# Performance work log

Measured on AMD Instinct MI355X. Metric: run time of the kernel, lower is better.

The kernel has to match this reference:

```python
import jax, jax.numpy as jnp
import numpy as np

N, E, H, L = 20000, 640000, 128, 3
IN_NODE, IN_EDGE = 128, 128


def _ln(x):
    m = jnp.mean(x, -1, keepdims=True)
    v = jnp.mean((x - m) ** 2, -1, keepdims=True)
    return (x - m) / jnp.sqrt(v + 1e-5)


def _multi_aggr(msg, dst, n):
    # PyG MultiAggregation(['mean','std','max','min']) -> concat on feature dim
    cnt = jax.ops.segment_sum(jnp.ones((msg.shape[0],), msg.dtype), dst, n)
    denom = jnp.maximum(cnt, 1.0)[:, None]
    mean = jax.ops.segment_sum(msg, dst, n) / denom
    mean2 = jax.ops.segment_sum(msg * msg, dst, n) / denom
    std = jnp.sqrt(jax.nn.relu(mean2 - mean * mean) + 1e-5)  # PyG StdAggregation
    has = (cnt > 0)[:, None]
    mx = jnp.where(has, jax.ops.segment_max(msg, dst, n), 0.0)
    mn = jnp.where(has, jax.ops.segment_min(msg, dst, n), 0.0)
    return jnp.concatenate([mean, std, mx, mn], axis=-1)  # [n, 4H]


def _pna(h, src, dst, ea, W1, b1, W2, b2, W3, b3, W4, b4, Wd, bd, n):
    # flow='source_to_target': j = src = edge_index[0], i = dst = edge_index[1]
    x1 = jax.nn.silu(h @ W1 + b1)  # lin1 -> x_j
    z = jax.nn.silu(h @ W2 + b2)   # lin2 -> z_i
    msg = z[dst] * x1[src] * ea    # message = z_i * x_j * edge_attr
    ret_node = _multi_aggr(msg, dst, n) @ Wd + bd
    ret_edge = jax.nn.silu(h @ W3 + b3)[src] * jax.nn.silu(h @ W4 + b4)[dst] * ea
    return ret_node, ret_edge


def _gnn(x, edge_index, edge_attr, Wn, bn, We, be, W1, b1, W2, b2, W3, b3, W4, b4,
         Wd, bd, Wnd1, bnd1, Wnd2, bnd2, Wed1, bed1, Wed2, bed2):
    n = x.shape[0]
    h = Wn.shape[1]
    src, dst = edge_index[0], edge_index[1]
    inv = jnp.concatenate([jnp.ones((h // 2,), x.dtype), -jnp.ones(((h + 1) // 2,), x.dtype)])
    hidden = x @ Wn + bn
    in_ea = edge_attr
    ea = edge_attr @ We + be
    for i in range(W1.shape[0]):
        hn = _ln(hidden)
        rn1, re1 = _pna(hn, src, dst, ea, W1[i], b1[i], W2[i], b2[i], W3[i], b3[i], W4[i], b4[i], Wd[i], bd[i], n)
        rn2, re2 = _pna(hn, dst, src, inv * ea, W1[i], b1[i], W2[i], b2[i], W3[i], b3[i], W4[i], b4[i], Wd[i], bd[i], n)
        hidden = hidden + rn1 + rn2
        ea = ea + re1 + inv * re2
    node_pred = x + 0.01 * (jax.nn.silu(_ln(hidden) @ Wnd1 + bnd1) @ Wnd2 + bnd2)
    edge_pred = in_ea + 0.01 * (jax.nn.silu(_ln(ea) @ Wed1 + bed1) @ Wed2 + bed2)
    return node_pred, edge_pred


def setup_inputs() -> dict:
    key = jax.random.key(0)
    ks = jax.random.split(key, 20)
    g = lambda k, s, sc=0.05: jax.random.normal(k, s, jnp.float32) * sc
    return {
        "x": g(ks[0], (N, IN_NODE), 1.0),
        "edge_attr": g(ks[1], (E, IN_EDGE), 1.0),
        "Wn": g(ks[2], (IN_NODE, H)), "bn": jnp.zeros((H,), jnp.float32),
        "We": g(ks[3], (IN_EDGE, H)), "be": jnp.zeros((H,), jnp.float32),
        "W1": g(ks[4], (L, H, H)), "b1": jnp.zeros((L, H), jnp.float32),
        "W2": g(ks[5], (L, H, H)), "b2": jnp.zeros((L, H), jnp.float32),
        "W3": g(ks[6], (L, H, H)), "b3": jnp.zeros((L, H), jnp.float32),
        "W4": g(ks[7], (L, H, H)), "b4": jnp.zeros((L, H), jnp.float32),
        "Wd": g(ks[8], (L, 4 * H, H)), "bd": jnp.zeros((L, H), jnp.float32),
        "Wnd1": g(ks[9], (H, H)), "bnd1": jnp.zeros((H,), jnp.float32),
        "Wnd2": g(ks[10], (H, IN_NODE)), "bnd2": jnp.zeros((IN_NODE,), jnp.float32),
        "Wed1": g(ks[11], (H, H)), "bed1": jnp.zeros((H,), jnp.float32),
        "Wed2": g(ks[12], (H, IN_EDGE)), "bed2": jnp.zeros((IN_EDGE,), jnp.float32),
        "edge_index": jax.random.randint(ks[13], (2, E), 0, N),
    }


def reference(x, edge_attr, Wn, bn, We, be, W1, b1, W2, b2, W3, b3, W4, b4, Wd, bd,
              Wnd1, bnd1, Wnd2, bnd2, Wed1, bed1, Wed2, bed2, edge_index):
    return _gnn(x, edge_index, edge_attr, Wn, bn, We, be, W1, b1, W2, b2, W3, b3,
                W4, b4, Wd, bd, Wnd1, bnd1, Wnd2, bnd2, Wed1, bed1, Wed2, bed2)
```

## Files before the change

kernel.cpp:

```cpp
#include <hip/hip_runtime.h>
#include <cstdint>
#include <cstddef>

typedef __attribute__((ext_vector_type(8))) short short8x;
typedef __attribute__((ext_vector_type(4))) float f32x4;

static constexpr int NN = 20000;
static constexpr int EE = 640000;
static constexpr int NT_E = EE / 128;

#define DEVI __device__ __forceinline__

DEVI float b2f(uint16_t u){ union{uint32_t i; float f;} x; x.i = (uint32_t)u<<16; return x.f; }
DEVI uint16_t f2b(float f){ union{float f; uint32_t i;} x; x.f=f; uint32_t i=x.i;
  return (uint16_t)((i + 0x7FFFu + ((i>>16)&1u))>>16); }
DEVI float silu_f(float v){ return v / (1.f + __expf(-v)); }

DEVI uint4 pack8(float4 a, float4 b){
  union{uint16_t u[8]; uint4 q;} pk;
  pk.u[0]=f2b(a.x); pk.u[1]=f2b(a.y); pk.u[2]=f2b(a.z); pk.u[3]=f2b(a.w);
  pk.u[4]=f2b(b.x); pk.u[5]=f2b(b.y); pk.u[6]=f2b(b.z); pk.u[7]=f2b(b.w);
  return pk.q;
}
DEVI uint2 pack4(float4 a){
  union{uint16_t u[4]; uint2 q;} pk;
  pk.u[0]=f2b(a.x); pk.u[1]=f2b(a.y); pk.u[2]=f2b(a.z); pk.u[3]=f2b(a.w);
  return pk.q;
}
DEVI float4 unpk4(uint2 v){
  return (float4){ b2f((uint16_t)(v.x & 0xFFFFu)), b2f((uint16_t)(v.x >> 16)),
                   b2f((uint16_t)(v.y & 0xFFFFu)), b2f((uint16_t)(v.y >> 16)) };
}
DEVI short8x pk_frag(float4 a, float4 b){
  union{uint16_t u[8]; short8x s;} pk;
  pk.u[0]=f2b(a.x); pk.u[1]=f2b(a.y); pk.u[2]=f2b(a.z); pk.u[3]=f2b(a.w);
  pk.u[4]=f2b(b.x); pk.u[5]=f2b(b.y); pk.u[6]=f2b(b.z); pk.u[7]=f2b(b.w);
  return pk.s;
}

template<typename EAT>
DEVI void load8e(const EAT* base, size_t row, int col8, float4& a, float4& b){
  if constexpr (sizeof(EAT)==2){
    uint4 v = *(const uint4*)((const uint16_t*)base + row*128 + col8);
    a = (float4){b2f((uint16_t)(v.x&0xFFFFu)), b2f((uint16_t)(v.x>>16)),
                 b2f((uint16_t)(v.y&0xFFFFu)), b2f((uint16_t)(v.y>>16))};
    b = (float4){b2f((uint16_t)(v.z&0xFFFFu)), b2f((uint16_t)(v.z>>16)),
                 b2f((uint16_t)(v.w&0xFFFFu)), b2f((uint16_t)(v.w>>16))};
  } else {
    const float* f = (const float*)base + row*128 + col8;
    a = *(const float4*)f; b = *(const float4*)(f+4);
  }
}
template<typename EAT>
DEVI void store4e(EAT* base, size_t idx, float4 v){
  if constexpr (sizeof(EAT)==2) *(uint2*)((uint16_t*)base + idx) = pack4(v);
  else *(float4*)((float*)base + idx) = v;
}
template<typename EAT>
DEVI float4 ld4e(const EAT* base, size_t idx){
  if constexpr (sizeof(EAT)==2) return unpk4(*(const uint2*)((const uint16_t*)base + idx));
  else return *(const float4*)((const float*)base + idx);
}

DEVI void ln8(float4& a, float4& b){
  float s = a.x+a.y+a.z+a.w + b.x+b.y+b.z+b.w;
  float q = a.x*a.x+a.y*a.y+a.z*a.z+a.w*a.w + b.x*b.x+b.y*b.y+b.z*b.z+b.w*b.w;
#pragma unroll
  for (int d=1; d<16; d<<=1){ s += __shfl_xor(s,d); q += __shfl_xor(q,d); }
  float m = s * 0.0078125f;
  float rstd = rsqrtf(fmaxf(q*0.0078125f - m*m, 0.f) + 1e-5f);
  a.x=(a.x-m)*rstd; a.y=(a.y-m)*rstd; a.z=(a.z-m)*rstd; a.w=(a.w-m)*rstd;
  b.x=(b.x-m)*rstd; b.y=(b.y-m)*rstd; b.z=(b.z-m)*rstd; b.w=(b.w-m)*rstd;
}

template<int AF32, int LNA, int EPI, int SILU>
__global__ __launch_bounds__(256) void gemm_node(
    const void* Ap, const uint16_t* __restrict__ Wt,
    const float* __restrict__ bias, float bias_scale,
    int M, int K,
    uint16_t* outb, float* outf,
    const float* __restrict__ resid, float resid_scale)
{
  __shared__ uint16_t Als[128*136];
  __shared__ uint16_t Wls[128*136];
  const int t = threadIdx.x;
  const int row0 = blockIdx.x * 128;
  const int w = t >> 6, l = t & 63;
  const int lr = l & 15, lk = (l>>4)*8;

  f32x4 acc[2][8];
#pragma unroll
  for (int a=0;a<2;a++)
#pragma unroll
    for(int b=0;b<8;b++) acc[a][b] = (f32x4){0.f,0.f,0.f,0.f};

  for (int kc = 0; kc < K; kc += 128){
#pragma unroll
    for (int i=0;i<8;i++){
      int c = t + i*256;
      int r = c >> 4, k8 = (c & 15)*8;
      int gr = row0 + r;
      if (AF32){
        float4 a = {0.f,0.f,0.f,0.f}, b = {0.f,0.f,0.f,0.f};
        if (gr < M){
          const float* Af = (const float*)Ap + (size_t)gr*K + kc + k8;
          a = *(const float4*)Af; b = *(const float4*)(Af + 4);
        }
        if (LNA) ln8(a, b);
        *(uint4*)(&Als[r*136 + k8]) = pack8(a, b);
      } else {
        uint4 v = {0u,0u,0u,0u};
        if (gr < M) v = *(const uint4*)((const uint16_t*)Ap + (size_t)gr*K + kc + k8);
        *(uint4*)(&Als[r*136 + k8]) = v;
      }
    }
#pragma unroll
    for (int i=0;i<8;i++){
      int c = t + i*256;
      int r = c >> 4, k8 = (c & 15)*8;
      *(uint4*)(&Wls[r*136 + k8]) = *(const uint4*)(Wt + (size_t)r*K + kc + k8);
    }
    __syncthreads();
#pragma unroll
    for (int kt=0; kt<4; ++kt){
      int kb = kt*32 + lk;
      short8x bfr[8];
#pragma unroll
      for (int c16=0;c16<8;c16++) bfr[c16] = *(const short8x*)(&Wls[(c16*16+lr)*136 + kb]);
#pragma unroll
      for (int r16=0;r16<2;r16++){
        short8x afr = *(const short8x*)(&Als[(w*32 + r16*16 + lr)*136 + kb]);
#pragma unroll
        for (int c16=0;c16<8;c16++)
          acc[r16][c16] = __builtin_amdgcn_mfma_f32_16x16x32_bf16(bfr[c16], afr, acc[r16][c16], 0,0,0);
      }
    }
    __syncthreads();
  }

  float4 bbv[8];
#pragma unroll
  for (int c16=0;c16<8;c16++){
    float4 b4 = *(const float4*)(bias + c16*16 + (l>>4)*4);
    bbv[c16] = (float4){b4.x*bias_scale, b4.y*bias_scale, b4.z*bias_scale, b4.w*bias_scale};
  }
#pragma unroll
  for (int r16=0;r16<2;r16++){
    int row = row0 + w*32 + r16*16 + lr;
    if (row >= M) continue;
#pragma unroll
    for (int c16=0;c16<8;c16++){
      int colb = c16*16 + (l>>4)*4;
      float4 v = (float4){acc[r16][c16][0]+bbv[c16].x, acc[r16][c16][1]+bbv[c16].y,
                          acc[r16][c16][2]+bbv[c16].z, acc[r16][c16][3]+bbv[c16].w};
      if (SILU){ v.x=silu_f(v.x); v.y=silu_f(v.y); v.z=silu_f(v.z); v.w=silu_f(v.w); }
      size_t o = (size_t)row*128 + colb;
      if (EPI==0)      *(uint2*)(outb + o) = pack4(v);
      else if (EPI==1) *(float4*)(outf + o) = v;
      else if (EPI==2){ float4 old = *(const float4*)(outf + o);
        *(float4*)(outf + o) = (float4){old.x+v.x, old.y+v.y, old.z+v.z, old.w+v.w}; }
      else { float4 r = *(const float4*)(resid + o);
        *(float4*)(outf + o) = (float4){r.x+resid_scale*v.x, r.y+resid_scale*v.y,
                                        r.z+resid_scale*v.z, r.w+resid_scale*v.w}; }
    }
  }
}

__global__ __launch_bounds__(256) void proj4(
    const float* __restrict__ hidden, const uint16_t* __restrict__ Wt4,
    const float* __restrict__ b0p, const float* __restrict__ b1p,
    const float* __restrict__ b2p, const float* __restrict__ b3p,
    uint16_t* o0, uint16_t* o1, uint16_t* o2, uint16_t* o3, int M)
{
  __shared__ uint16_t Als[128*136];
  __shared__ uint16_t Wls[2][128*136];
  const int t = threadIdx.x;
  const int row0 = blockIdx.x * 128;
  const int w = t >> 6, l = t & 63;
  const int lr = l & 15, lk = (l>>4)*8;

#pragma unroll
  for (int i=0;i<8;i++){
    int c = t + i*256;
    int r = c >> 4, k8 = (c & 15)*8;
    int gr = row0 + r;
    float4 a = {0.f,0.f,0.f,0.f}, b = {0.f,0.f,0.f,0.f};
    if (gr < M){
      const float* Af = hidden + (size_t)gr*128 + k8;
      a = *(const float4*)Af; b = *(const float4*)(Af + 4);
    }
    ln8(a, b);
    *(uint4*)(&Als[r*136 + k8]) = pack8(a, b);
  }
#pragma unroll
  for (int i=0;i<8;i++){
    int c = t + i*256;
    int r = c >> 4, k8 = (c & 15)*8;
    *(uint4*)(&Wls[0][r*136 + k8]) = *(const uint4*)(Wt4 + (size_t)r*128 + k8);
  }
  __syncthreads();

#pragma unroll
  for (int p=0; p<4; ++p){
    if (p < 3){
#pragma unroll
      for (int i=0;i<8;i++){
        int c = t + i*256;
        int r = c >> 4, k8 = (c & 15)*8;
        *(uint4*)(&Wls[(p+1)&1][r*136 + k8]) =
          *(const uint4*)(Wt4 + (size_t)(p+1)*16384 + (size_t)r*128 + k8);
      }
    }
    f32x4 acc[2][8];
#pragma unroll
    for (int a=0;a<2;a++)
#pragma unroll
      for(int b=0;b<8;b++) acc[a][b] = (f32x4){0.f,0.f,0.f,0.f};
#pragma unroll
    for (int kt=0; kt<4; ++kt){
      int kb = kt*32 + lk;
      short8x bfr[8];
#pragma unroll
      for (int c16=0;c16<8;c16++) bfr[c16] = *(const short8x*)(&Wls[p&1][(c16*16+lr)*136 + kb]);
#pragma unroll
      for (int r16=0;r16<2;r16++){
        short8x afr = *(const short8x*)(&Als[(w*32 + r16*16 + lr)*136 + kb]);
#pragma unroll
        for (int c16=0;c16<8;c16++)
          acc[r16][c16] = __builtin_amdgcn_mfma_f32_16x16x32_bf16(bfr[c16], afr, acc[r16][c16], 0,0,0);
      }
    }
    const float* bp = (p==0)?b0p:(p==1)?b1p:(p==2)?b2p:b3p;
    uint16_t* op = (p==0)?o0:(p==1)?o1:(p==2)?o2:o3;
#pragma unroll
    for (int r16=0;r16<2;r16++){
      int row = row0 + w*32 + r16*16 + lr;
      if (row >= M) continue;
#pragma unroll
      for (int c16=0;c16<8;c16++){
        int colb = c16*16 + (l>>4)*4;
        float4 b4 = *(const float4*)(bp + colb);
        float4 v = (float4){silu_f(acc[r16][c16][0]+b4.x), silu_f(acc[r16][c16][1]+b4.y),
                            silu_f(acc[r16][c16][2]+b4.z), silu_f(acc[r16][c16][3]+b4.w)};
        *(uint2*)(op + (size_t)row*128 + colb) = pack4(v);
      }
    }
    __syncthreads();
  }
}

template<typename EAT>
__global__ __launch_bounds__(256, 2) void enc_edge(
    const float* __restrict__ A, const uint16_t* __restrict__ Wt,
    const float* __restrict__ bias, EAT* __restrict__ out)
{
  const int t = threadIdx.x, w = t >> 6, l = t & 63;
  const int lr = l & 15, g = l >> 4;
  const size_t base = (size_t)blockIdx.x*128 + w*32;

  short8x fr[2][4];
#pragma unroll
  for (int r16=0;r16<2;r16++){
#pragma unroll
    for (int kt=0;kt<4;kt++){
      const float* Af = A + (base + r16*16 + lr)*128 + kt*32 + g*8;
      float4 a = *(const float4*)Af, b = *(const float4*)(Af + 4);
      fr[r16][kt] = pk_frag(a, b);
    }
  }
  f32x4 acc[2][8];
#pragma unroll
  for (int a=0;a<2;a++)
#pragma unroll
    for (int b=0;b<8;b++) acc[a][b] = (f32x4){0.f,0.f,0.f,0.f};
#pragma unroll
  for (int kt=0;kt<4;kt++){
#pragma unroll
    for (int c16=0;c16<8;c16++){
      short8x bfr = *(const short8x*)(Wt + (size_t)(c16*16+lr)*128 + kt*32 + g*8);
      acc[0][c16] = __builtin_amdgcn_mfma_f32_16x16x32_bf16(bfr, fr[0][kt], acc[0][c16], 0,0,0);
      acc[1][c16] = __builtin_amdgcn_mfma_f32_16x16x32_bf16(bfr, fr[1][kt], acc[1][c16], 0,0,0);
    }
  }
#pragma unroll
  for (int r16=0;r16<2;r16++){
    size_t row = base + r16*16 + lr;
#pragma unroll
    for (int c16=0;c16<8;c16++){
      int colb = c16*16 + g*4;
      float4 b4 = *(const float4*)(bias + colb);
      store4e(out, row*128 + colb,
        (float4){acc[r16][c16][0]+b4.x, acc[r16][c16][1]+b4.y,
                 acc[r16][c16][2]+b4.z, acc[r16][c16][3]+b4.w});
    }
  }
}

template<typename EAT>
__global__ __launch_bounds__(256, 2) void dec_edge(
    const EAT* ea, const float* __restrict__ eatt,
    const uint16_t* __restrict__ W1t, const uint16_t* __restrict__ W2t,
    const float* __restrict__ b1, const float* __restrict__ b2,
    float* outf)
{
  __shared__ uint16_t Pls[4][32*136];
  const int t = threadIdx.x, w = t >> 6, l = t & 63;
  const int lr = l & 15, g = l >> 4;
  uint16_t* Ps = &Pls[w][0];
  const size_t base = (size_t)blockIdx.x*128 + w*32;

  short8x fr[2][4];
#pragma unroll
  for (int r16=0;r16<2;r16++){
    float4 va[4][2];
    float s=0.f, q=0.f;
#pragma unroll
    for (int kt=0;kt<4;kt++){
      load8e(ea, base + r16*16 + lr, kt*32 + g*8, va[kt][0], va[kt][1]);
      float4 a = va[kt][0], b = va[kt][1];
      s += a.x+a.y+a.z+a.w + b.x+b.y+b.z+b.w;
      q += a.x*a.x+a.y*a.y+a.z*a.z+a.w*a.w + b.x*b.x+b.y*b.y+b.z*b.z+b.w*b.w;
    }
    s += __shfl_xor(s,16); q += __shfl_xor(q,16);
    s += __shfl_xor(s,32); q += __shfl_xor(q,32);
    float m = s*0.0078125f;
    float rstd = rsqrtf(fmaxf(q*0.0078125f - m*m, 0.f) + 1e-5f);
#pragma unroll
    for (int kt=0;kt<4;kt++){
      float4 a = va[kt][0], b = va[kt][1];
      a.x=(a.x-m)*rstd; a.y=(a.y-m)*rstd; a.z=(a.z-m)*rstd; a.w=(a.w-m)*rstd;
      b.x=(b.x-m)*rstd; b.y=(b.y-m)*rstd; b.z=(b.z-m)*rstd; b.w=(b.w-m)*rstd;
      fr[r16][kt] = pk_frag(a, b);
    }
  }
  f32x4 acc[2][8];
#pragma unroll
  for (int a=0;a<2;a++)
#pragma unroll
    for (int b=0;b<8;b++) acc[a][b] = (f32x4){0.f,0.f,0.f,0.f};
#pragma unroll
  for (int kt=0;kt<4;kt++){
#pragma unroll
    for (int c16=0;c16<8;c16++){
      short8x bfr = *(const short8x*)(W1t + (size_t)(c16*16+lr)*128 + kt*32 + g*8);
      acc[0][c16] = __builtin_amdgcn_mfma_f32_16x16x32_bf16(fr[0][kt], bfr, acc[0][c16], 0,0,0);
      acc[1][c16] = __builtin_amdgcn_mfma_f32_16x16x32_bf16(fr[1][kt], bfr, acc[1][c16], 0,0,0);
    }
  }
#pragma unroll
  for (int c16=0;c16<8;c16++){
    float bb = b1[c16*16+lr];
#pragma unroll
    for (int r16=0;r16<2;r16++)
#pragma unroll
      for (int j=0;j<4;j++)
        Ps[(r16*16 + g*4 + j)*136 + c16*16 + lr] = f2b(silu_f(acc[r16][c16][j] + bb));
  }
  f32x4 acc2[2][8];
#pragma unroll
  for (int a=0;a<2;a++)
#pragma unroll
    for (int b=0;b<8;b++) acc2[a][b] = (f32x4){0.f,0.f,0.f,0.f};
#pragma unroll
  for (int kt=0;kt<4;kt++){
    short8x a0 = *(const short8x*)(Ps + (0*16 + lr)*136 + kt*32 + g*8);
    short8x a1 = *(const short8x*)(Ps + (1*16 + lr)*136 + kt*32 + g*8);
#pragma unroll
    for (int c16=0;c16<8;c16++){
      short8x bfr = *(const short8x*)(W2t + (size_t)(c16*16+lr)*128 + kt*32 + g*8);
      acc2[0][c16] = __builtin_amdgcn_mfma_f32_16x16x32_bf16(bfr, a0, acc2[0][c16], 0,0,0);
      acc2[1][c16] = __builtin_amdgcn_mfma_f32_16x16x32_bf16(bfr, a1, acc2[1][c16], 0,0,0);
    }
  }
#pragma unroll
  for (int r16=0;r16<2;r16++){
    size_t row = base + r16*16 + lr;
    float4 et[8];
#pragma unroll
    for (int c16=0;c16<8;c16++) et[c16] = *(const float4*)(eatt + row*128 + c16*16 + g*4);
#pragma unroll
    for (int c16=0;c16<8;c16++){
      int colb = c16*16 + g*4;
      float4 bb = *(const float4*)(b2 + colb);
      *(float4*)(outf + row*128 + colb) =
        (float4){et[c16].x + 0.01f*(acc2[r16][c16][0]+bb.x),
                 et[c16].y + 0.01f*(acc2[r16][c16][1]+bb.y),
                 et[c16].z + 0.01f*(acc2[r16][c16][2]+bb.z),
                 et[c16].w + 0.01f*(acc2[r16][c16][3]+bb.w)};
    }
  }
}

template<typename EAT, int INV, int EUPD, int ACCUM>
__global__ __launch_bounds__(128) void agg_kernel(
    const EAT* ea, EAT* ea_out,
    const uint16_t* __restrict__ x1, const uint16_t* __restrict__ z,
    const uint16_t* __restrict__ h3, const uint16_t* __restrict__ h4,
    const int* __restrict__ eids, const int* __restrict__ ptr,
    const int* __restrict__ other, uint16_t* stats)
{
  __shared__ int se[128];
  __shared__ int so[128];
  __shared__ float red[4][4][128];
  const int i = blockIdx.x, t = threadIdx.x;
  const int g = t >> 5, q = t & 31;
  const int f0 = q*4;
  float4 zi = unpk4(*(const uint2*)(z + (size_t)i*128 + f0));
  float4 h3i = {0,0,0,0}, h4i = {0,0,0,0};
  if (EUPD){
    h3i = unpk4(*(const uint2*)(h3 + (size_t)i*128 + f0));
    h4i = unpk4(*(const uint2*)(h4 + (size_t)i*128 + f0));
  }
  const int beg = ptr[i], end = ptr[i+1];
  float4 s={0,0,0,0}, s2={0,0,0,0};
  float4 mx={-3.4e38f,-3.4e38f,-3.4e38f,-3.4e38f}, mn={3.4e38f,3.4e38f,3.4e38f,3.4e38f};
  for (int jb = beg; jb < end; jb += 128){
    int cn = min(128, end - jb);
    if (t < cn){ int e = eids[jb+t]; se[t] = e; so[t] = other[e]; }
    __syncthreads();
#pragma unroll 2
    for (int jj = g; jj < cn; jj += 4){
      int e = se[jj], o = so[jj];
      float4 xo = unpk4(*(const uint2*)(x1 + (size_t)o*128 + f0));
      float4 ev = ld4e(ea, (size_t)e*128 + f0);
      float4 m = (float4){zi.x*xo.x*ev.x, zi.y*xo.y*ev.y, zi.z*xo.z*ev.z, zi.w*xo.w*ev.w};
      if (INV){ if (q >= 16){ m.x=-m.x; m.y=-m.y; m.z=-m.z; m.w=-m.w; } }
      s.x+=m.x; s.y+=m.y; s.z+=m.z; s.w+=m.w;
      s2.x+=m.x*m.x; s2.y+=m.y*m.y; s2.z+=m.z*m.z; s2.w+=m.w*m.w;
      mx.x=fmaxf(mx.x,m.x); mx.y=fmaxf(mx.y,m.y); mx.z=fmaxf(mx.z,m.z); mx.w=fmaxf(mx.w,m.w);
      mn.x=fminf(mn.x,m.x); mn.y=fminf(mn.y,m.y); mn.z=fminf(mn.z,m.z); mn.w=fminf(mn.w,m.w);
      if (EUPD){
        float4 h3o = unpk4(*(const uint2*)(h3 + (size_t)o*128 + f0));
        float4 h4o = unpk4(*(const uint2*)(h4 + (size_t)o*128 + f0));
        store4e(ea_out, (size_t)e*128 + f0,
          (float4){ev.x*(1.f + h3o.x*h4i.x + h3i.x*h4o.x),
                   ev.y*(1.f + h3o.y*h4i.y + h3i.y*h4o.y),
                   ev.z*(1.f + h3o.z*h4i.z + h3i.z*h4o.z),
                   ev.w*(1.f + h3o.w*h4i.w + h3i.w*h4o.w)});
      }
    }
    __syncthreads();
  }
  *(float4*)(&red[g][0][f0]) = s;
  *(float4*)(&red[g][1][f0]) = s2;
  *(float4*)(&red[g][2][f0]) = mx;
  *(float4*)(&red[g][3][f0]) = mn;
  __syncthreads();
  float fs = red[0][0][t]+red[1][0][t]+red[2][0][t]+red[3][0][t];
  float fq = red[0][1][t]+red[1][1][t]+red[2][1][t]+red[3][1][t];
  float fmx = fmaxf(fmaxf(red[0][2][t],red[1][2][t]), fmaxf(red[2][2][t],red[3][2][t]));
  float fmn = fminf(fminf(red[0][3][t],red[1][3][t]), fminf(red[2][3][t],red[3][3][t]));
  int cnt = end - beg;
  float dn = cnt > 0 ? 1.f/(float)cnt : 1.f;
  float mean = fs*dn, m2 = fq*dn;
  float sd = sqrtf(fmaxf(m2 - mean*mean, 0.f) + 1e-5f);
  if (cnt == 0){ fmx = 0.f; fmn = 0.f; }
  size_t o0 = (size_t)i*512 + t;
  if (ACCUM){
    stats[o0    ] = f2b(b2f(stats[o0    ]) + mean);
    stats[o0+128] = f2b(b2f(stats[o0+128]) + sd);
    stats[o0+256] = f2b(b2f(stats[o0+256]) + fmx);
    stats[o0+384] = f2b(b2f(stats[o0+384]) + fmn);
  } else {
    stats[o0]=f2b(mean); stats[o0+128]=f2b(sd); stats[o0+256]=f2b(fmx); stats[o0+384]=f2b(fmn);
  }
}

__global__ void count_deg(const int* __restrict__ ei, int* cnt_src, int* cnt_dst){
  int e = blockIdx.x*256 + threadIdx.x;
  if (e < EE){
    atomicAdd(&cnt_src[ei[e]], 1);
    atomicAdd(&cnt_dst[ei[EE+e]], 1);
  }
}

__global__ __launch_bounds__(1024) void scan20k(const int* __restrict__ cnt, int* ptr){
  __shared__ int buf[1024];
  constexpr int C = 20;
  int t = threadIdx.x;
  int base = t*C;
  int loc[C];
  int sum = 0;
#pragma unroll
  for (int j=0;j<C;j++){
    int idx = base+j;
    int v = (idx < NN) ? cnt[idx] : 0;
    loc[j] = sum; sum += v;
  }
  buf[t] = sum;
  __syncthreads();
  for (int sft=1; sft<1024; sft<<=1){
    int add = (t>=sft) ? buf[t-sft] : 0;
    __syncthreads();
    buf[t] += add;
    __syncthreads();
  }
  int excl = buf[t] - sum;
#pragma unroll
  for (int j=0;j<C;j++){
    int idx = base+j;
    if (idx < NN) ptr[idx] = excl + loc[j];
  }
  if (t == 1023) ptr[NN] = buf[1023];
}

__global__ void init_cursor(const int* p1, int* c1, const int* p2, int* c2, int n){
  int i = blockIdx.x*256 + threadIdx.x;
  if (i < n){ c1[i] = p1[i]; c2[i] = p2[i]; }
}

__global__ void scatter_edges(const int* __restrict__ ei, int* cur_src, int* cur_dst,
                              int* eid_src, int* eid_dst){
  int e = blockIdx.x*256 + threadIdx.x;
  if (e < EE){
    int s = ei[e], d = ei[EE+e];
    eid_src[atomicAdd(&cur_src[s],1)] = e;
    eid_dst[atomicAdd(&cur_dst[d],1)] = e;
  }
}

__global__ void transpose_w(const float* __restrict__ W, uint16_t* __restrict__ Wt,
                            int K, int total, int ostride, int ooff){
  int idx = blockIdx.x*256 + threadIdx.x;
  if (idx < total){
    int per = K*128;
    int m = idx / per, r = idx - m*per;
    int k = r >> 7, c = r & 127;
    Wt[(size_t)m*ostride + ooff + (size_t)c*K + k] = f2b(W[idx]);
  }
}

extern "C" void kernel_launch(void* const* d_in, const int* in_sizes, int n_in,
                              void* d_out, int out_size, void* d_ws, size_t ws_size,
                              hipStream_t stream)
{
  const float* x    = (const float*)d_in[0];
  const float* eatt = (const float*)d_in[1];
  const float* Wn   = (const float*)d_in[2];
  const float* bn   = (const float*)d_in[3];
  const float* We   = (const float*)d_in[4];
  const float* be   = (const float*)d_in[5];
  const float* W1   = (const float*)d_in[6];
  const float* b1   = (const float*)d_in[7];
  const float* W2   = (const float*)d_in[8];
  const float* b2   = (const float*)d_in[9];
  const float* W3   = (const float*)d_in[10];
  const float* b3   = (const float*)d_in[11];
  const float* W4   = (const float*)d_in[12];
  const float* b4   = (const float*)d_in[13];
  const float* Wd   = (const float*)d_in[14];
  const float* bd   = (const float*)d_in[15];
  const float* Wnd1 = (const float*)d_in[16];
  const float* bnd1 = (const float*)d_in[17];
  const float* Wnd2 = (const float*)d_in[18];
  const float* bnd2 = (const float*)d_in[19];
  const float* Wed1 = (const float*)d_in[20];
  const float* bed1 = (const float*)d_in[21];
  const float* Wed2 = (const float*)d_in[22];
  const float* bed2 = (const float*)d_in[23];
  const int* ei     = (const int*)d_in[24];

  float* out_node = (float*)d_out;
  float* out_edge = out_node + (size_t)NN*128;

  char* p = (char*)d_ws;
  auto alloc = [&](size_t bytes)->char*{
    char* r = p; p += (bytes + 255) & ~(size_t)255; return r; };

  float*    hidden = (float*)   alloc((size_t)NN*128*4);
  uint16_t* x1b    = (uint16_t*)alloc((size_t)NN*128*2);
  uint16_t* zb     = (uint16_t*)alloc((size_t)NN*128*2);
  uint16_t* h3b    = (uint16_t*)alloc((size_t)NN*128*2);
  uint16_t* h4b    = (uint16_t*)alloc((size_t)NN*128*2);
  uint16_t* stats  = (uint16_t*)alloc((size_t)NN*512*2);
  int* cnt_src = (int*)alloc((size_t)NN*4);
  int* cnt_dst = (int*)alloc((size_t)NN*4);
  int* ptr_src = (int*)alloc((size_t)(NN+1)*4);
  int* ptr_dst = (int*)alloc((size_t)(NN+1)*4);
  int* cur_src = (int*)alloc((size_t)NN*4);
  int* cur_dst = (int*)alloc((size_t)NN*4);
  int* eid_src = (int*)alloc((size_t)EE*4);
  int* eid_dst = (int*)alloc((size_t)EE*4);
  uint16_t* WT  = (uint16_t*)alloc((size_t)294912*2);
  uint16_t* wp4 = (uint16_t*)alloc((size_t)3*65536*2);

  uint16_t* wnT   = WT;
  uint16_t* weT   = WT + 16384;
  uint16_t* wdT   = WT + 32768;
  uint16_t* wnd1T = WT + 229376;
  uint16_t* wnd2T = WT + 245760;
  uint16_t* wed1T = WT + 262144;
  uint16_t* wed2T = WT + 278528;

  size_t used = (size_t)(p - (char*)d_ws);
  bool ea16ok = (ws_size >= used + (size_t)EE*128*2 + 512);
  uint16_t* ea16 = nullptr;
  if (ea16ok) ea16 = (uint16_t*)alloc((size_t)EE*128*2);
  float* eaf = out_edge;

  hipMemsetAsync(cnt_src, 0, (size_t)NN*4, stream);
  hipMemsetAsync(cnt_dst, 0, (size_t)NN*4, stream);
  count_deg<<<(EE+255)/256, 256, 0, stream>>>(ei, cnt_src, cnt_dst);
  scan20k<<<1, 1024, 0, stream>>>(cnt_src, ptr_src);
  scan20k<<<1, 1024, 0, stream>>>(cnt_dst, ptr_dst);
  init_cursor<<<(NN+255)/256, 256, 0, stream>>>(ptr_src, cur_src, ptr_dst, cur_dst, NN);
  scatter_edges<<<(EE+255)/256, 256, 0, stream>>>(ei, cur_src, cur_dst, eid_src, eid_dst);

  transpose_w<<<64, 256, 0, stream>>>(Wn, wnT, 128, 16384, 16384, 0);
  transpose_w<<<64, 256, 0, stream>>>(We, weT, 128, 16384, 16384, 0);
  transpose_w<<<192, 256, 0, stream>>>(W1, wp4, 128, 49152, 65536, 0);
  transpose_w<<<192, 256, 0, stream>>>(W2, wp4, 128, 49152, 65536, 16384);
  transpose_w<<<192, 256, 0, stream>>>(W3, wp4, 128, 49152, 65536, 32768);
  transpose_w<<<192, 256, 0, stream>>>(W4, wp4, 128, 49152, 65536, 49152);
  transpose_w<<<768, 256, 0, stream>>>(Wd, wdT, 512, 196608, 65536, 0);
  transpose_w<<<64, 256, 0, stream>>>(Wnd1, wnd1T, 128, 16384, 16384, 0);
  transpose_w<<<64, 256, 0, stream>>>(Wnd2, wnd2T, 128, 16384, 16384, 0);
  transpose_w<<<64, 256, 0, stream>>>(Wed1, wed1T, 128, 16384, 16384, 0);
  transpose_w<<<64, 256, 0, stream>>>(Wed2, wed2T, 128, 16384, 16384, 0);

  const int gN = (NN+127)/128;

  gemm_node<1,0,1,0><<<gN, 256, 0, stream>>>(x, wnT, bn, 1.f, NN, 128, nullptr, hidden, nullptr, 0.f);

  if (ea16ok){
    enc_edge<uint16_t><<<NT_E, 256, 0, stream>>>(eatt, weT, be, ea16);
    for (int lyr = 0; lyr < 3; ++lyr){
      proj4<<<gN, 256, 0, stream>>>(hidden, wp4 + (size_t)lyr*65536,
                                    b1 + lyr*128, b2 + lyr*128, b3 + lyr*128, b4 + lyr*128,
                                    x1b, zb, h3b, h4b, NN);
      agg_kernel<uint16_t,1,0,0><<<NN, 128, 0, stream>>>(ea16, nullptr, x1b, zb, nullptr, nullptr,
                                                         eid_src, ptr_src, ei + EE, stats);
      agg_kernel<uint16_t,0,1,1><<<NN, 128, 0, stream>>>(ea16, ea16, x1b, zb, h3b, h4b,
                                                         eid_dst, ptr_dst, ei, stats);
      gemm_node<0,0,2,0><<<gN, 256, 0, stream>>>(stats, wdT + lyr*65536, bd + lyr*128, 2.f,
                                                 NN, 512, nullptr, hidden, nullptr, 0.f);
    }
  } else {
    enc_edge<float><<<NT_E, 256, 0, stream>>>(eatt, weT, be, eaf);
    for (int lyr = 0; lyr < 3; ++lyr){
      proj4<<<gN, 256, 0, stream>>>(hidden, wp4 + (size_t)lyr*65536,
                                    b1 + lyr*128, b2 + lyr*128, b3 + lyr*128, b4 + lyr*128,
                                    x1b, zb, h3b, h4b, NN);
      agg_kernel<float,1,0,0><<<NN, 128, 0, stream>>>(eaf, nullptr, x1b, zb, nullptr, nullptr,
                                                      eid_src, ptr_src, ei + EE, stats);
      agg_kernel<float,0,1,1><<<NN, 128, 0, stream>>>(eaf, eaf, x1b, zb, h3b, h4b,
                                                      eid_dst, ptr_dst, ei, stats);
      gemm_node<0,0,2,0><<<gN, 256, 0, stream>>>(stats, wdT + lyr*65536, bd + lyr*128, 2.f,
                                                 NN, 512, nullptr, hidden, nullptr, 0.f);
    }
  }

  gemm_node<1,1,0,1><<<gN, 256, 0, stream>>>(hidden, wnd1T, bnd1, 1.f, NN, 128, x1b, nullptr, nullptr, 0.f);
  gemm_node<0,0,3,0><<<gN, 256, 0, stream>>>(x1b, wnd2T, bnd2, 1.f, NN, 128, nullptr, out_node, x, 0.01f);

  if (ea16ok)
    dec_edge<uint16_t><<<NT_E, 256, 0, stream>>>(ea16, eatt, wed1T, wed2T, bed1, bed2, out_edge);
  else
    dec_edge<float><<<NT_E, 256, 0, stream>>>(eaf, eatt, wed1T, wed2T, bed1, bed2, out_edge);
}
```

Baseline: 1.401 ms.

## Persistent prefetching edge encoder, wider aggregation blocks, fused weight transposes and cursor init

The edge encoder becomes a persistent kernel over 1000 blocks that prefetches the next tile's inputs into registers while the current tile runs its MFMAs, with bias hoisted out of the loop. Aggregation blocks double to 256 threads (8 edge groups), and the final reduction is split so half the threads compute mean/std and half max/min. The eleven weight-transpose launches merge into one kernel, and cursor initialisation folds into the scan. The edge decoder also issues its residual loads early. The aim is lower launch overhead, better latency hiding and more parallelism in the gather-bound aggregation, at the cost of higher register use and more shared memory per aggregation block.

```diff
diff --git a/kernel.cpp b/kernel.cpp
--- a/kernel.cpp
+++ b/kernel.cpp
@@ -256,43 +256,65 @@
 {
   const int t = threadIdx.x, w = t >> 6, l = t & 63;
   const int lr = l & 15, g = l >> 4;
-  const size_t base = (size_t)blockIdx.x*128 + w*32;
-
-  short8x fr[2][4];
-#pragma unroll
-  for (int r16=0;r16<2;r16++){
+
+  float4 bbv[8];
+#pragma unroll
+  for (int c16=0;c16<8;c16++) bbv[c16] = *(const float4*)(bias + c16*16 + g*4);
+
+  int tile = blockIdx.x;
+  float4 va[16];
+#pragma unroll
+  for (int r16=0;r16<2;r16++)
 #pragma unroll
     for (int kt=0;kt<4;kt++){
-      const float* Af = A + (base + r16*16 + lr)*128 + kt*32 + g*8;
-      float4 a = *(const float4*)Af, b = *(const float4*)(Af + 4);
-      fr[r16][kt] = pk_frag(a, b);
-    }
-  }
-  f32x4 acc[2][8];
-#pragma unroll
-  for (int a=0;a<2;a++)
-#pragma unroll
-    for (int b=0;b<8;b++) acc[a][b] = (f32x4){0.f,0.f,0.f,0.f};
-#pragma unroll
-  for (int kt=0;kt<4;kt++){
-#pragma unroll
-    for (int c16=0;c16<8;c16++){
-      short8x bfr = *(const short8x*)(Wt + (size_t)(c16*16+lr)*128 + kt*32 + g*8);
-      acc[0][c16] = __builtin_amdgcn_mfma_f32_16x16x32_bf16(bfr, fr[0][kt], acc[0][c16], 0,0,0);
-      acc[1][c16] = __builtin_amdgcn_mfma_f32_16x16x32_bf16(bfr, fr[1][kt], acc[1][c16], 0,0,0);
-    }
-  }
-#pragma unroll
-  for (int r16=0;r16<2;r16++){
-    size_t row = base + r16*16 + lr;
-#pragma unroll
-    for (int c16=0;c16<8;c16++){
-      int colb = c16*16 + g*4;
-      float4 b4 = *(const float4*)(bias + colb);
-      store4e(out, row*128 + colb,
-        (float4){acc[r16][c16][0]+b4.x, acc[r16][c16][1]+b4.y,
-                 acc[r16][c16][2]+b4.z, acc[r16][c16][3]+b4.w});
-    }
+      const float* Af = A + ((size_t)tile*128 + w*32 + r16*16 + lr)*128 + kt*32 + g*8;
+      va[r16*8+kt*2]   = *(const float4*)Af;
+      va[r16*8+kt*2+1] = *(const float4*)(Af + 4);
+    }
+  while (tile < NT_E){
+    short8x fr[2][4];
+#pragma unroll
+    for (int r16=0;r16<2;r16++)
+#pragma unroll
+      for (int kt=0;kt<4;kt++)
+        fr[r16][kt] = pk_frag(va[r16*8+kt*2], va[r16*8+kt*2+1]);
+    int next = tile + (int)gridDim.x;
+    if (next < NT_E){
+#pragma unroll
+      for (int r16=0;r16<2;r16++)
+#pragma unroll
+        for (int kt=0;kt<4;kt++){
+          const float* Af = A + ((size_t)next*128 + w*32 + r16*16 + lr)*128 + kt*32 + g*8;
+          va[r16*8+kt*2]   = *(const float4*)Af;
+          va[r16*8+kt*2+1] = *(const float4*)(Af + 4);
+        }
+    }
+    f32x4 acc[2][8];
+#pragma unroll
+    for (int a=0;a<2;a++)
+#pragma unroll
+      for (int b=0;b<8;b++) acc[a][b] = (f32x4){0.f,0.f,0.f,0.f};
+#pragma unroll
+    for (int kt=0;kt<4;kt++){
+#pragma unroll
+      for (int c16=0;c16<8;c16++){
+        short8x bfr = *(const short8x*)(Wt + (size_t)(c16*16+lr)*128 + kt*32 + g*8);
+        acc[0][c16] = __builtin_amdgcn_mfma_f32_16x16x32_bf16(bfr, fr[0][kt], acc[0][c16], 0,0,0);
+        acc[1][c16] = __builtin_amdgcn_mfma_f32_16x16x32_bf16(bfr, fr[1][kt], acc[1][c16], 0,0,0);
+      }
+    }
+#pragma unroll
+    for (int r16=0;r16<2;r16++){
+      size_t row = (size_t)tile*128 + w*32 + r16*16 + lr;
+#pragma unroll
+      for (int c16=0;c16<8;c16++){
+        int colb = c16*16 + g*4;
+        store4e(out, row*128 + colb,
+          (float4){acc[r16][c16][0]+bbv[c16].x, acc[r16][c16][1]+bbv[c16].y,
+                   acc[r16][c16][2]+bbv[c16].z, acc[r16][c16][3]+bbv[c16].w});
+      }
+    }
+    tile = next;
   }
 }
 
@@ -309,6 +331,15 @@
   uint16_t* Ps = &Pls[w][0];
   const size_t base = (size_t)blockIdx.x*128 + w*32;
 
+  float4 et[16];
+#pragma unroll
+  for (int r16=0;r16<2;r16++){
+    size_t row = base + r16*16 + lr;
+#pragma unroll
+    for (int c16=0;c16<8;c16++)
+      et[r16*8+c16] = *(const float4*)(eatt + row*128 + c16*16 + g*4);
+  }
+
   short8x fr[2][4];
 #pragma unroll
   for (int r16=0;r16<2;r16++){
@@ -375,24 +406,22 @@
 #pragma unroll
   for (int r16=0;r16<2;r16++){
     size_t row = base + r16*16 + lr;
-    float4 et[8];
-#pragma unroll
-    for (int c16=0;c16<8;c16++) et[c16] = *(const float4*)(eatt + row*128 + c16*16 + g*4);
 #pragma unroll
     for (int c16=0;c16<8;c16++){
       int colb = c16*16 + g*4;
       float4 bb = *(const float4*)(b2 + colb);
+      float4 e = et[r16*8+c16];
       *(float4*)(outf + row*128 + colb) =
-        (float4){et[c16].x + 0.01f*(acc2[r16][c16][0]+bb.x),
-                 et[c16].y + 0.01f*(acc2[r16][c16][1]+bb.y),
-                 et[c16].z + 0.01f*(acc2[r16][c16][2]+bb.z),
-                 et[c16].w + 0.01f*(acc2[r16][c16][3]+bb.w)};
+        (float4){e.x + 0.01f*(acc2[r16][c16][0]+bb.x),
+                 e.y + 0.01f*(acc2[r16][c16][1]+bb.y),
+                 e.z + 0.01f*(acc2[r16][c16][2]+bb.z),
+                 e.w + 0.01f*(acc2[r16][c16][3]+bb.w)};
     }
   }
 }
 
 template<typename EAT, int INV, int EUPD, int ACCUM>
-__global__ __launch_bounds__(128) void agg_kernel(
+__global__ __launch_bounds__(256) void agg_kernel(
     const EAT* ea, EAT* ea_out,
     const uint16_t* __restrict__ x1, const uint16_t* __restrict__ z,
     const uint16_t* __restrict__ h3, const uint16_t* __restrict__ h4,
@@ -401,7 +430,7 @@
 {
   __shared__ int se[128];
   __shared__ int so[128];
-  __shared__ float red[4][4][128];
+  __shared__ float red[8][4][128];
   const int i = blockIdx.x, t = threadIdx.x;
   const int g = t >> 5, q = t & 31;
   const int f0 = q*4;
@@ -418,8 +447,8 @@
     int cn = min(128, end - jb);
     if (t < cn){ int e = eids[jb+t]; se[t] = e; so[t] = other[e]; }
     __syncthreads();
-#pragma unroll 2
-    for (int jj = g; jj < cn; jj += 4){
+#pragma unroll 4
+    for (int jj = g; jj < cn; jj += 8){
       int e = se[jj], o = so[jj];
       float4 xo = unpk4(*(const uint2*)(x1 + (size_t)o*128 + f0));
       float4 ev = ld4e(ea, (size_t)e*128 + f0);
@@ -446,23 +475,35 @@
   *(float4*)(&red[g][2][f0]) = mx;
   *(float4*)(&red[g][3][f0]) = mn;
   __syncthreads();
-  float fs = red[0][0][t]+red[1][0][t]+red[2][0][t]+red[3][0][t];
-  float fq = red[0][1][t]+red[1][1][t]+red[2][1][t]+red[3][1][t];
-  float fmx = fmaxf(fmaxf(red[0][2][t],red[1][2][t]), fmaxf(red[2][2][t],red[3][2][t]));
-  float fmn = fminf(fminf(red[0][3][t],red[1][3][t]), fminf(red[2][3][t],red[3][3][t]));
   int cnt = end - beg;
-  float dn = cnt > 0 ? 1.f/(float)cnt : 1.f;
-  float mean = fs*dn, m2 = fq*dn;
-  float sd = sqrtf(fmaxf(m2 - mean*mean, 0.f) + 1e-5f);
-  if (cnt == 0){ fmx = 0.f; fmn = 0.f; }
-  size_t o0 = (size_t)i*512 + t;
-  if (ACCUM){
-    stats[o0    ] = f2b(b2f(stats[o0    ]) + mean);
-    stats[o0+128] = f2b(b2f(stats[o0+128]) + sd);
-    stats[o0+256] = f2b(b2f(stats[o0+256]) + fmx);
-    stats[o0+384] = f2b(b2f(stats[o0+384]) + fmn);
+  if (t < 128){
+    int f = t;
+    float fs=0.f, fq=0.f;
+#pragma unroll
+    for (int gg=0; gg<8; ++gg){ fs += red[gg][0][f]; fq += red[gg][1][f]; }
+    float dn = cnt > 0 ? 1.f/(float)cnt : 1.f;
+    float mean = fs*dn;
+    float sd = sqrtf(fmaxf(fq*dn - mean*mean, 0.f) + 1e-5f);
+    size_t o0 = (size_t)i*512 + f;
+    if (ACCUM){
+      stats[o0    ] = f2b(b2f(stats[o0    ]) + mean);
+      stats[o0+128] = f2b(b2f(stats[o0+128]) + sd);
+    } else {
+      stats[o0] = f2b(mean); stats[o0+128] = f2b(sd);
+    }
   } else {
-    stats[o0]=f2b(mean); stats[o0+128]=f2b(sd); stats[o0+256]=f2b(fmx); stats[o0+384]=f2b(fmn);
+    int f = t - 128;
+    float fmx=-3.4e38f, fmn=3.4e38f;
+#pragma unroll
+    for (int gg=0; gg<8; ++gg){ fmx = fmaxf(fmx, red[gg][2][f]); fmn = fminf(fmn, red[gg][3][f]); }
+    if (cnt == 0){ fmx = 0.f; fmn = 0.f; }
+    size_t o0 = (size_t)i*512 + f;
+    if (ACCUM){
+      stats[o0+256] = f2b(b2f(stats[o0+256]) + fmx);
+      stats[o0+384] = f2b(b2f(stats[o0+384]) + fmn);
+    } else {
+      stats[o0+256] = f2b(fmx); stats[o0+384] = f2b(fmn);
+    }
   }
 }
 
@@ -474,7 +515,7 @@
   }
 }
 
-__global__ __launch_bounds__(1024) void scan20k(const int* __restrict__ cnt, int* ptr){
+__global__ __launch_bounds__(1024) void scan20k(const int* __restrict__ cnt, int* ptr, int* cur){
   __shared__ int buf[1024];
   constexpr int C = 20;
   int t = threadIdx.x;
@@ -499,14 +540,9 @@
 #pragma unroll
   for (int j=0;j<C;j++){
     int idx = base+j;
-    if (idx < NN) ptr[idx] = excl + loc[j];
+    if (idx < NN){ int v = excl + loc[j]; ptr[idx] = v; cur[idx] = v; }
   }
   if (t == 1023) ptr[NN] = buf[1023];
-}
-
-__global__ void init_cursor(const int* p1, int* c1, const int* p2, int* c2, int n){
-  int i = blockIdx.x*256 + threadIdx.x;
-  if (i < n){ c1[i] = p1[i]; c2[i] = p2[i]; }
 }
 
 __global__ void scatter_edges(const int* __restrict__ ei, int* cur_src, int* cur_dst,
@@ -519,15 +555,21 @@
   }
 }
 
-__global__ void transpose_w(const float* __restrict__ W, uint16_t* __restrict__ Wt,
-                            int K, int total, int ostride, int ooff){
+struct TD { const float* s; uint16_t* d; int K; int ostride; int ooff; int cum; };
+struct TPack { TD td[11]; };
+__global__ __launch_bounds__(256) void transpose_all(TPack P, int total){
   int idx = blockIdx.x*256 + threadIdx.x;
-  if (idx < total){
-    int per = K*128;
-    int m = idx / per, r = idx - m*per;
-    int k = r >> 7, c = r & 127;
-    Wt[(size_t)m*ostride + ooff + (size_t)c*K + k] = f2b(W[idx]);
-  }
+  if (idx >= total) return;
+  int s = 0;
+#pragma unroll
+  for (int k=0;k<11;k++) s += (idx >= P.td[k].cum) ? 1 : 0;
+  int start = (s==0) ? 0 : P.td[s-1].cum;
+  int local = idx - start;
+  const TD& D = P.td[s];
+  int per = D.K*128;
+  int m = local / per, r = local - m*per;
+  int k = r >> 7, c = r & 127;
+  D.d[(size_t)m*D.ostride + D.ooff + (size_t)c*D.K + k] = f2b(D.s[local]);
 }
 
 extern "C" void kernel_launch(void* const* d_in, const int* in_sizes, int n_in,
@@ -601,49 +643,57 @@
   hipMemsetAsync(cnt_src, 0, (size_t)NN*4, stream);
   hipMemsetAsync(cnt_dst, 0, (size_t)NN*4, stream);
   count_deg<<<(EE+255)/256, 256, 0, stream>>>(ei, cnt_src, cnt_dst);
-  scan20k<<<1, 1024, 0, stream>>>(cnt_src, ptr_src);
-  scan20k<<<1, 1024, 0, stream>>>(cnt_dst, ptr_dst);
-  init_cursor<<<(NN+255)/256, 256, 0, stream>>>(ptr_src, cur_src, ptr_dst, cur_dst, NN);
+  scan20k<<<1, 1024, 0, stream>>>(cnt_src, ptr_src, cur_src);
+  scan20k<<<1, 1024, 0, stream>>>(cnt_dst, ptr_dst, cur_dst);
   scatter_edges<<<(EE+255)/256, 256, 0, stream>>>(ei, cur_src, cur_dst, eid_src, eid_dst);
 
-  transpose_w<<<64, 256, 0, stream>>>(Wn, wnT, 128, 16384, 16384, 0);
-  transpose_w<<<64, 256, 0, stream>>>(We, weT, 128, 16384, 16384, 0);
-  transpose_w<<<192, 256, 0, stream>>>(W1, wp4, 128, 49152, 65536, 0);
-  transpose_w<<<192, 256, 0, stream>>>(W2, wp4, 128, 49152, 65536, 16384);
-  transpose_w<<<192, 256, 0, stream>>>(W3, wp4, 128, 49152, 65536, 32768);
-  transpose_w<<<192, 256, 0, stream>>>(W4, wp4, 128, 49152, 65536, 49152);
-  transpose_w<<<768, 256, 0, stream>>>(Wd, wdT, 512, 196608, 65536, 0);
-  transpose_w<<<64, 256, 0, stream>>>(Wnd1, wnd1T, 128, 16384, 16384, 0);
-  transpose_w<<<64, 256, 0, stream>>>(Wnd2, wnd2T, 128, 16384, 16384, 0);
-  transpose_w<<<64, 256, 0, stream>>>(Wed1, wed1T, 128, 16384, 16384, 0);
-  transpose_w<<<64, 256, 0, stream>>>(Wed2, wed2T, 128, 16384, 16384, 0);
+  {
+    TPack P;
+    int cum = 0;
+    auto seg = [&](int idx, const float* s, uint16_t* d, int K, int total, int ostride, int ooff){
+      cum += total;
+      P.td[idx] = TD{s, d, K, ostride, ooff, cum};
+    };
+    seg(0,  Wn,   wnT,   128, 16384,  16384, 0);
+    seg(1,  We,   weT,   128, 16384,  16384, 0);
+    seg(2,  W1,   wp4,   128, 49152,  65536, 0);
+    seg(3,  W2,   wp4,   128, 49152,  65536, 16384);
+    seg(4,  W3,   wp4,   128, 49152,  65536, 32768);
+    seg(5,  W4,   wp4,   128, 49152,  65536, 49152);
+    seg(6,  Wd,   wdT,   512, 196608, 65536, 0);
+    seg(7,  Wnd1, wnd1T, 128, 16384,  16384, 0);
+    seg(8,  Wnd2, wnd2T, 128, 16384,  16384, 0);
+    seg(9,  Wed1, wed1T, 128, 16384,  16384, 0);
+    seg(10, Wed2, wed2T, 128, 16384,  16384, 0);
+    transpose_all<<<(cum+255)/256, 256, 0, stream>>>(P, cum);
+  }
 
   const int gN = (NN+127)/128;
 
   gemm_node<1,0,1,0><<<gN, 256, 0, stream>>>(x, wnT, bn, 1.f, NN, 128, nullptr, hidden, nullptr, 0.f);
 
   if (ea16ok){
-    enc_edge<uint16_t><<<NT_E, 256, 0, stream>>>(eatt, weT, be, ea16);
+    enc_edge<uint16_t><<<1000, 256, 0, stream>>>(eatt, weT, be, ea16);
     for (int lyr = 0; lyr < 3; ++lyr){
       proj4<<<gN, 256, 0, stream>>>(hidden, wp4 + (size_t)lyr*65536,
                                     b1 + lyr*128, b2 + lyr*128, b3 + lyr*128, b4 + lyr*128,
                                     x1b, zb, h3b, h4b, NN);
-      agg_kernel<uint16_t,1,0,0><<<NN, 128, 0, stream>>>(ea16, nullptr, x1b, zb, nullptr, nullptr,
+      agg_kernel<uint16_t,1,0,0><<<NN, 256, 0, stream>>>(ea16, nullptr, x1b, zb, nullptr, nullptr,
                                                          eid_src, ptr_src, ei + EE, stats);
-      agg_kernel<uint16_t,0,1,1><<<NN, 128, 0, stream>>>(ea16, ea16, x1b, zb, h3b, h4b,
+      agg_kernel<uint16_t,0,1,1><<<NN, 256, 0, stream>>>(ea16, ea16, x1b, zb, h3b, h4b,
                                                          eid_dst, ptr_dst, ei, stats);
       gemm_node<0,0,2,0><<<gN, 256, 0, stream>>>(stats, wdT + lyr*65536, bd + lyr*128, 2.f,
                                                  NN, 512, nullptr, hidden, nullptr, 0.f);
     }
   } else {
-    enc_edge<float><<<NT_E, 256, 0, stream>>>(eatt, weT, be, eaf);
+    enc_edge<float><<<1000, 256, 0, stream>>>(eatt, weT, be, eaf);
     for (int lyr = 0; lyr < 3; ++lyr){
       proj4<<<gN, 256, 0, stream>>>(hidden, wp4 + (size_t)lyr*65536,
                                     b1 + lyr*128, b2 + lyr*128, b3 + lyr*128, b4 + lyr*128,
                                     x1b, zb, h3b, h4b, NN);
-      agg_kernel<float,1,0,0><<<NN, 128, 0, stream>>>(eaf, nullptr, x1b, zb, nullptr, nullptr,
+      agg_kernel<float,1,0,0><<<NN, 256, 0, stream>>>(eaf, nullptr, x1b, zb, nullptr, nullptr,
                                                       eid_src, ptr_src, ei + EE, stats);
-      agg_kernel<float,0,1,1><<<NN, 128, 0, stream>>>(eaf, eaf, x1b, zb, h3b, h4b,
+      agg_kernel<float,0,1,1><<<NN, 256, 0, stream>>>(eaf, eaf, x1b, zb, h3b, h4b,
                                                       eid_dst, ptr_dst, ei, stats);
       gemm_node<0,0,2,0><<<gN, 256, 0, stream>>>(stats, wdT + lyr*65536, bd + lyr*128, 2.f,
                                                  NN, 512, nullptr, hidden, nullptr, 0.f);
```

Measured after the change: 1.450 ms. 1.03x slower.
